# Kernel optimization log

Measured on AMD Instinct MI355X. Metric: run time of the kernel, lower is better.

Reference implementation:

```python
import jax, jax.numpy as jnp
import numpy as np

B, N, C, K, OUT = 4, 16384, 64, 16, 128
BN_EPS = 1e-5


def setup_inputs() -> dict:
    key = jax.random.key(0)
    ks = jax.random.split(key, 6)
    feature = jax.random.normal(ks[0], (B, C, N), dtype=jnp.float32)
    neigh_index = jax.random.randint(ks[1], (B * N, K), 0, B * N)
    permatrix = jnp.zeros((1,), dtype=jnp.float32)  # unused by forward
    # Conv1d(in_c, in_c, kernel_size=1, bias=False) -> weight [C, C]
    W_mlp = jax.random.normal(ks[2], (C, C), dtype=jnp.float32) / np.sqrt(C).astype(np.float32)
    # Linear(in_c, out_c) -> weight [OUT, C], bias [OUT]
    W_conv = jax.random.normal(ks[3], (OUT, C), dtype=jnp.float32) / np.sqrt(C).astype(np.float32)
    b_conv = jax.random.normal(ks[4], (OUT,), dtype=jnp.float32) * 0.01
    gamma = jnp.ones((OUT,), dtype=jnp.float32)
    beta = jnp.zeros((OUT,), dtype=jnp.float32)
    return {
        "feature": feature,
        "neigh_index": neigh_index,
        "permatrix": permatrix,
        "W_mlp": W_mlp,
        "W_conv": W_conv,
        "b_conv": b_conv,
        "gamma": gamma,
        "beta": beta,
    }


def reference(feature, neigh_index, permatrix, W_mlp, W_conv, b_conv, gamma, beta):
    bsize, feats, num_pts = feature.shape
    # [B, C, N] -> [B*N, C]
    flat = feature.transpose(0, 2, 1).reshape(bsize * num_pts, feats)
    # irregular gather: [B*N, k, C]
    spirals = flat[neigh_index]
    # 1x1 conv over channels: einsum with mlp weight [C_out=C, C_in=C]
    scores = jnp.einsum("nkc,dc->nkd", spirals, W_mlp)  # [B*N, k, C]
    # softmax over channel dim (torch dim=1 on [BN, C, k] layout)
    attn = jax.nn.softmax(scores, axis=-1)
    # attention pooling over the k neighbors -> [B*N, C]
    pooled = jnp.sum(attn * spirals, axis=1)
    # Linear: [B*N, OUT]
    out = pooled @ W_conv.T + b_conv
    # [B, OUT, N]
    out = out.reshape(bsize, num_pts, -1).transpose(0, 2, 1)
    # BatchNorm1d (training-mode batch statistics) over (batch, points) per channel
    mean = jnp.mean(out, axis=(0, 2), keepdims=True)
    var = jnp.var(out, axis=(0, 2), keepdims=True)
    out = (out - mean) * jax.lax.rsqrt(var + BN_EPS)
    out = out * gamma[None, :, None] + beta[None, :, None]
    return out
```

## Files before the change

### kernel.cpp

```cpp
#include <hip/hip_runtime.h>
#include <cstdint>

#define NPTS   16384
#define BATCH  4
#define BNP    65536
#define CIN    64
#define KNB    16
#define COUT   128
#define BN_EPS 1e-5f

typedef __attribute__((ext_vector_type(8))) short     short8;
typedef __attribute__((ext_vector_type(4))) float     f32x4;
typedef __attribute__((ext_vector_type(2))) unsigned  u32x2;
typedef __attribute__((ext_vector_type(4))) int       i32x4;

__device__ __forceinline__ unsigned short f2bf(float f) {
    unsigned u = __float_as_uint(f);
    u += 0x7FFFu + ((u >> 16) & 1u);
    return (unsigned short)(u >> 16);
}
__device__ __forceinline__ float bf2f(unsigned short h) {
    return __uint_as_float(((unsigned)h) << 16);
}

__global__ __launch_bounds__(256) void k_prep(const float* __restrict__ feat,
                                              unsigned short* __restrict__ fb,
                                              const float* __restrict__ Wm,
                                              const float* __restrict__ Wc,
                                              unsigned short* __restrict__ wmb,
                                              unsigned short* __restrict__ wcb)
{
    if (blockIdx.x == 1024) {
        #pragma unroll
        for (int i = threadIdx.x; i < CIN * CIN; i += 256)       wmb[i] = f2bf(Wm[i]);
        #pragma unroll
        for (int i = threadIdx.x; i < COUT * CIN; i += 256)      wcb[i] = f2bf(Wc[i]);
        return;
    }
    __shared__ float t[CIN][CIN + 1];
    int blk = blockIdx.x;
    int b   = blk >> 8;
    int n0  = (blk & 255) << 6;
    int sub = threadIdx.x >> 6, lane = threadIdx.x & 63;
    const float* fp = feat + (size_t)b * CIN * NPTS;
    #pragma unroll
    for (int r = 0; r < CIN; r += 4) {
        int c = r + sub;
        t[c][lane] = fp[(size_t)c * NPTS + n0 + lane];
    }
    __syncthreads();
    unsigned short* ob = fb + (size_t)(b * NPTS + n0) * CIN;
    #pragma unroll
    for (int r = 0; r < CIN; r += 4) {
        int x = r + sub;
        ob[(size_t)x * CIN + lane] = f2bf(t[lane][x]);
    }
}

__global__ __launch_bounds__(256, 2) void k_main(
    const unsigned short* __restrict__ fb,
    const int* __restrict__ nidx,
    const unsigned short* __restrict__ wmb,
    const unsigned short* __restrict__ wcb,
    float* __restrict__ out)
{
    __shared__ __align__(16) unsigned short plds[4][2][1152];

    const int tid  = threadIdx.x;
    const int wv   = tid >> 6;
    const int lane = tid & 63;
    const int ptc  = lane & 15;
    const int qg   = lane >> 4;
    const int p4   = ptc * 4;

    short8 wmF[4][2];
    #pragma unroll
    for (int mt = 0; mt < 4; ++mt)
        #pragma unroll
        for (int ks = 0; ks < 2; ++ks)
            wmF[mt][ks] = *(const short8*)&wmb[(size_t)(mt * 16 + ptc) * CIN + qg * 8 + ks * 32];
    short8 wcF[8][2];
    #pragma unroll
    for (int mt = 0; mt < 8; ++mt)
        #pragma unroll
        for (int ks = 0; ks < 2; ++ks)
            wcF[mt][ks] = *(const short8*)&wcb[(size_t)(mt * 16 + ptc) * CIN + qg * 8 + ks * 32];

    f32x4 acc2[8];
    #pragma unroll
    for (int i = 0; i < 8; ++i) acc2[i] = (f32x4){0.f, 0.f, 0.f, 0.f};

    const int g = blockIdx.x * 4 + wv;

    i32x4 iv = *(const i32x4*)(nidx + (size_t)g * 256 + lane * 4);

    short8 rb0[4], rb1[4];
    u32x2  svr[4][4];
    int    rid[4];
    #pragma unroll
    for (int kk = 0; kk < 4; ++kk) {
        int id = __shfl(iv[kk], p4);
        rid[kk] = id;
        const unsigned short* gp = fb + (size_t)id * CIN;
        rb0[kk] = *(const short8*)(gp + qg * 8);
        rb1[kk] = *(const short8*)(gp + 32 + qg * 8);
        #pragma unroll
        for (int mt = 0; mt < 4; ++mt)
            svr[kk][mt] = *(const u32x2*)(gp + mt * 16 + qg * 4);
    }

    #pragma unroll
    for (int p = 0; p < 8; ++p) {
        const int sA = (2 * p) & 3;
        const int sB = sA + 1;

        f32x4 zero4 = (f32x4){0.f, 0.f, 0.f, 0.f};
        f32x4 a1A[4], a1B[4];
        #pragma unroll
        for (int mt = 0; mt < 4; ++mt) {
            f32x4 t0 = __builtin_amdgcn_mfma_f32_16x16x32_bf16(wmF[mt][0], rb0[sA], zero4, 0, 0, 0);
            a1A[mt]  = __builtin_amdgcn_mfma_f32_16x16x32_bf16(wmF[mt][1], rb1[sA], t0,    0, 0, 0);
        }
        #pragma unroll
        for (int mt = 0; mt < 4; ++mt) {
            f32x4 t0 = __builtin_amdgcn_mfma_f32_16x16x32_bf16(wmF[mt][0], rb0[sB], zero4, 0, 0, 0);
            a1B[mt]  = __builtin_amdgcn_mfma_f32_16x16x32_bf16(wmF[mt][1], rb1[sB], t0,    0, 0, 0);
        }

        if (p < 6) {
            int idA = __shfl(iv[sA], p4 + ((2 * p + 4) >> 2));
            int idB = __shfl(iv[sB], p4 + ((2 * p + 5) >> 2));
            rid[sA] = idA;
            rid[sB] = idB;
            const unsigned short* gA = fb + (size_t)idA * CIN;
            const unsigned short* gB = fb + (size_t)idB * CIN;
            rb0[sA] = *(const short8*)(gA + qg * 8);
            rb1[sA] = *(const short8*)(gA + 32 + qg * 8);
            rb0[sB] = *(const short8*)(gB + qg * 8);
            rb1[sB] = *(const short8*)(gB + 32 + qg * 8);
        }

        float ssA = 0.f, ssB = 0.f;
        #pragma unroll
        for (int mt = 0; mt < 4; ++mt)
            #pragma unroll
            for (int r = 0; r < 4; ++r) {
                float xA = __expf(a1A[mt][r]);
                float xB = __expf(a1B[mt][r]);
                a1A[mt][r] = xA;  ssA += xA;
                a1B[mt][r] = xB;  ssB += xB;
            }
        ssA += __shfl_xor(ssA, 16);
        ssB += __shfl_xor(ssB, 16);
        ssA += __shfl_xor(ssA, 32);
        ssB += __shfl_xor(ssB, 32);
        float invA = __builtin_amdgcn_rcpf(ssA);
        float invB = __builtin_amdgcn_rcpf(ssB);

        #pragma unroll
        for (int mt = 0; mt < 4; ++mt) {
            u32x2 svA = svr[sA][mt], svB = svr[sB][mt];
            unsigned loA = svA[0], hiA = svA[1];
            unsigned loB = svB[0], hiB = svB[1];
            float pA0 = bf2f((unsigned short)loA)         * (a1A[mt][0] * invA);
            float pA1 = bf2f((unsigned short)(loA >> 16)) * (a1A[mt][1] * invA);
            float pA2 = bf2f((unsigned short)hiA)         * (a1A[mt][2] * invA);
            float pA3 = bf2f((unsigned short)(hiA >> 16)) * (a1A[mt][3] * invA);
            float pB0 = bf2f((unsigned short)loB)         * (a1B[mt][0] * invB);
            float pB1 = bf2f((unsigned short)(loB >> 16)) * (a1B[mt][1] * invB);
            float pB2 = bf2f((unsigned short)hiB)         * (a1B[mt][2] * invB);
            float pB3 = bf2f((unsigned short)(hiB >> 16)) * (a1B[mt][3] * invB);
            unsigned wA0 = ((__float_as_uint(pA0) + 0x8000u) >> 16) |
                           ((__float_as_uint(pA1) + 0x8000u) & 0xFFFF0000u);
            unsigned wA1 = ((__float_as_uint(pA2) + 0x8000u) >> 16) |
                           ((__float_as_uint(pA3) + 0x8000u) & 0xFFFF0000u);
            unsigned wB0 = ((__float_as_uint(pB0) + 0x8000u) >> 16) |
                           ((__float_as_uint(pB1) + 0x8000u) & 0xFFFF0000u);
            unsigned wB1 = ((__float_as_uint(pB2) + 0x8000u) >> 16) |
                           ((__float_as_uint(pB3) + 0x8000u) & 0xFFFF0000u);
            *(u32x2*)&plds[wv][0][ptc * 72 + mt * 16 + qg * 4] = (u32x2){wA0, wA1};
            *(u32x2*)&plds[wv][1][ptc * 72 + mt * 16 + qg * 4] = (u32x2){wB0, wB1};
        }

        if (p < 6) {
            const unsigned short* gA = fb + (size_t)rid[sA] * CIN;
            const unsigned short* gB = fb + (size_t)rid[sB] * CIN;
            #pragma unroll
            for (int mt = 0; mt < 4; ++mt) {
                svr[sA][mt] = *(const u32x2*)(gA + mt * 16 + qg * 4);
                svr[sB][mt] = *(const u32x2*)(gB + mt * 16 + qg * 4);
            }
        }

        short8 b2A0 = *(const short8*)&plds[wv][0][ptc * 72 +      qg * 8];
        short8 b2A1 = *(const short8*)&plds[wv][0][ptc * 72 + 32 + qg * 8];
        short8 b2B0 = *(const short8*)&plds[wv][1][ptc * 72 +      qg * 8];
        short8 b2B1 = *(const short8*)&plds[wv][1][ptc * 72 + 32 + qg * 8];

        #pragma unroll
        for (int mt = 0; mt < 8; ++mt) {
            acc2[mt] = __builtin_amdgcn_mfma_f32_16x16x32_bf16(wcF[mt][0], b2A0, acc2[mt], 0, 0, 0);
            acc2[mt] = __builtin_amdgcn_mfma_f32_16x16x32_bf16(wcF[mt][1], b2A1, acc2[mt], 0, 0, 0);
        }
        #pragma unroll
        for (int mt = 0; mt < 8; ++mt) {
            acc2[mt] = __builtin_amdgcn_mfma_f32_16x16x32_bf16(wcF[mt][0], b2B0, acc2[mt], 0, 0, 0);
            acc2[mt] = __builtin_amdgcn_mfma_f32_16x16x32_bf16(wcF[mt][1], b2B1, acc2[mt], 0, 0, 0);
        }
    }

    {
        int p0 = g * KNB;
        int b  = p0 >> 14;
        int nn = (p0 & (NPTS - 1)) + ptc;
        float* ob = out + (((size_t)b * COUT) << 14) + nn;
        #pragma unroll
        for (int mt = 0; mt < 8; ++mt)
            #pragma unroll
            for (int r = 0; r < 4; ++r)
                ob[((size_t)(mt * 16 + qg * 4 + r)) << 14] = acc2[mt][r];
    }
}

__global__ __launch_bounds__(256) void k_part(const float* __restrict__ out,
                                              float* __restrict__ part)
{
    int o = blockIdx.x >> 2, b = blockIdx.x & 3;
    const float4* p = (const float4*)(out + (((size_t)(b * COUT + o)) << 14));
    float s = 0.f, q = 0.f;
    for (int i = threadIdx.x; i < NPTS / 4; i += 256) {
        float4 v = p[i];
        s += (v.x + v.y) + (v.z + v.w);
        q += (v.x * v.x + v.y * v.y) + (v.z * v.z + v.w * v.w);
    }
    #pragma unroll
    for (int off = 32; off >= 1; off >>= 1) {
        s += __shfl_xor(s, off);
        q += __shfl_xor(q, off);
    }
    __shared__ float ls[4], lq[4];
    if ((threadIdx.x & 63) == 0) { ls[threadIdx.x >> 6] = s; lq[threadIdx.x >> 6] = q; }
    __syncthreads();
    if (threadIdx.x == 0) {
        part[blockIdx.x * 2]     = (ls[0] + ls[1]) + (ls[2] + ls[3]);
        part[blockIdx.x * 2 + 1] = (lq[0] + lq[1]) + (lq[2] + lq[3]);
    }
}

__global__ __launch_bounds__(256) void k_apply(float* __restrict__ out,
                                               const float* __restrict__ part,
                                               const float* __restrict__ gamma,
                                               const float* __restrict__ beta)
{
    __shared__ float sc[COUT], sh[COUT];
    int t = threadIdx.x;
    if (t < COUT) {
        float s = 0.f, q = 0.f;
        #pragma unroll
        for (int j = 0; j < 4; ++j) {
            s += part[(t * 4 + j) * 2];
            q += part[(t * 4 + j) * 2 + 1];
        }
        float mean = s * (1.0f / BNP);
        float var  = q * (1.0f / BNP) - mean * mean;
        float a = gamma[t] * rsqrtf(var + BN_EPS);
        sc[t] = a; sh[t] = beta[t] - mean * a;
    }
    __syncthreads();
    const int total4 = BATCH * COUT * NPTS / 4;
    for (long i = (long)blockIdx.x * 256 + t; i < total4; i += (long)gridDim.x * 256) {
        int ch = ((int)(i >> 12)) & 127;
        float4 v = ((float4*)out)[i];
        float a = sc[ch], b2 = sh[ch];
        v.x = fmaf(v.x, a, b2); v.y = fmaf(v.y, a, b2);
        v.z = fmaf(v.z, a, b2); v.w = fmaf(v.w, a, b2);
        ((float4*)out)[i] = v;
    }
}

extern "C" void kernel_launch(void* const* d_in, const int* in_sizes, int n_in,
                              void* d_out, int out_size, void* d_ws, size_t ws_size,
                              hipStream_t stream)
{
    const float* feat  = (const float*)d_in[0];
    const int*   nidx  = (const int*)  d_in[1];
    const float* Wm    = (const float*)d_in[3];
    const float* Wc    = (const float*)d_in[4];
    const float* gamma = (const float*)d_in[6];
    const float* beta  = (const float*)d_in[7];
    float* out = (float*)d_out;

    char* ws = (char*)d_ws;
    unsigned short* fb   = (unsigned short*)ws;
    float*          part = (float*)(ws + (size_t)BNP * CIN * 2);
    unsigned short* wmb  = (unsigned short*)(ws + (size_t)BNP * CIN * 2 + 4096);
    unsigned short* wcb  = wmb + CIN * CIN;

    k_prep <<<1025, 256, 0, stream>>>(feat, fb, Wm, Wc, wmb, wcb);
    k_main <<<1024, 256, 0, stream>>>(fb, nidx, wmb, wcb, out);
    k_part <<<512,  256, 0, stream>>>(out, part);
    k_apply<<<2048, 256, 0, stream>>>(out, part, gamma, beta);
}
```

Before: 165.5 us.

## Fuse BatchNorm statistics into main kernel via shuffle reduction and atomics

```diff
diff --git a/kernel.cpp b/kernel.cpp
--- a/kernel.cpp
+++ b/kernel.cpp
@@ -28,9 +28,11 @@
                                               const float* __restrict__ Wm,
                                               const float* __restrict__ Wc,
                                               unsigned short* __restrict__ wmb,
-                                              unsigned short* __restrict__ wcb)
+                                              unsigned short* __restrict__ wcb,
+                                              float* __restrict__ stat)
 {
     if (blockIdx.x == 1024) {
+        stat[threadIdx.x] = 0.f;
         #pragma unroll
         for (int i = threadIdx.x; i < CIN * CIN; i += 256)       wmb[i] = f2bf(Wm[i]);
         #pragma unroll
@@ -62,7 +64,8 @@
     const int* __restrict__ nidx,
     const unsigned short* __restrict__ wmb,
     const unsigned short* __restrict__ wcb,
-    float* __restrict__ out)
+    float* __restrict__ out,
+    float* __restrict__ stat)
 {
     __shared__ __align__(16) unsigned short plds[4][2][1152];
 
@@ -220,49 +223,37 @@
             for (int r = 0; r < 4; ++r)
                 ob[((size_t)(mt * 16 + qg * 4 + r)) << 14] = acc2[mt][r];
     }
-}
-
-__global__ __launch_bounds__(256) void k_part(const float* __restrict__ out,
-                                              float* __restrict__ part)
-{
-    int o = blockIdx.x >> 2, b = blockIdx.x & 3;
-    const float4* p = (const float4*)(out + (((size_t)(b * COUT + o)) << 14));
-    float s = 0.f, q = 0.f;
-    for (int i = threadIdx.x; i < NPTS / 4; i += 256) {
-        float4 v = p[i];
-        s += (v.x + v.y) + (v.z + v.w);
-        q += (v.x * v.x + v.y * v.y) + (v.z * v.z + v.w * v.w);
-    }
-    #pragma unroll
-    for (int off = 32; off >= 1; off >>= 1) {
-        s += __shfl_xor(s, off);
-        q += __shfl_xor(q, off);
-    }
-    __shared__ float ls[4], lq[4];
-    if ((threadIdx.x & 63) == 0) { ls[threadIdx.x >> 6] = s; lq[threadIdx.x >> 6] = q; }
-    __syncthreads();
-    if (threadIdx.x == 0) {
-        part[blockIdx.x * 2]     = (ls[0] + ls[1]) + (ls[2] + ls[3]);
-        part[blockIdx.x * 2 + 1] = (lq[0] + lq[1]) + (lq[2] + lq[3]);
-    }
+
+    #pragma unroll
+    for (int mt = 0; mt < 8; ++mt)
+        #pragma unroll
+        for (int r = 0; r < 4; ++r) {
+            float v = acc2[mt][r];
+            float s = v, q = v * v;
+            #pragma unroll
+            for (int m = 1; m <= 8; m <<= 1) {
+                s += __shfl_xor(s, m);
+                q += __shfl_xor(q, m);
+            }
+            if (ptc == 0) {
+                int ch = mt * 16 + qg * 4 + r;
+                atomicAdd(&stat[ch],        s);
+                atomicAdd(&stat[COUT + ch], q);
+            }
+        }
 }
 
 __global__ __launch_bounds__(256) void k_apply(float* __restrict__ out,
-                                               const float* __restrict__ part,
+                                               const float* __restrict__ stat,
                                                const float* __restrict__ gamma,
                                                const float* __restrict__ beta)
 {
     __shared__ float sc[COUT], sh[COUT];
     int t = threadIdx.x;
     if (t < COUT) {
-        float s = 0.f, q = 0.f;
-        #pragma unroll
-        for (int j = 0; j < 4; ++j) {
-            s += part[(t * 4 + j) * 2];
-            q += part[(t * 4 + j) * 2 + 1];
-        }
-        float mean = s * (1.0f / BNP);
-        float var  = q * (1.0f / BNP) - mean * mean;
+        float S = stat[t], Q = stat[COUT + t];
+        float mean = S * (1.0f / BNP);
+        float var  = Q * (1.0f / BNP) - mean * mean;
         float a = gamma[t] * rsqrtf(var + BN_EPS);
         sc[t] = a; sh[t] = beta[t] - mean * a;
     }
@@ -292,12 +283,11 @@
 
     char* ws = (char*)d_ws;
     unsigned short* fb   = (unsigned short*)ws;
-    float*          part = (float*)(ws + (size_t)BNP * CIN * 2);
-    unsigned short* wmb  = (unsigned short*)(ws + (size_t)BNP * CIN * 2 + 4096);
+    float*          stat = (float*)(ws + (size_t)BNP * CIN * 2);
+    unsigned short* wmb  = (unsigned short*)(ws + (size_t)BNP * CIN * 2 + 1024);
     unsigned short* wcb  = wmb + CIN * CIN;
 
-    k_prep <<<1025, 256, 0, stream>>>(feat, fb, Wm, Wc, wmb, wcb);
-    k_main <<<1024, 256, 0, stream>>>(fb, nidx, wmb, wcb, out);
-    k_part <<<512,  256, 0, stream>>>(out, part);
-    k_apply<<<2048, 256, 0, stream>>>(out, part, gamma, beta);
-}
+    k_prep <<<1025, 256, 0, stream>>>(feat, fb, Wm, Wc, wmb, wcb, stat);
+    k_main <<<1024, 256, 0, stream>>>(fb, nidx, wmb, wcb, out, stat);
+    k_apply<<<2048, 256, 0, stream>>>(out, stat, gamma, beta);
+}
```

Result: slower. 570.5 us (+244.7%).

## Fuse prep, main, stats and BN apply into one cooperative persistent kernel

Applied to the files above, without the earlier changes.

```diff
diff --git a/kernel.cpp b/kernel.cpp
--- a/kernel.cpp
+++ b/kernel.cpp
@@ -1,5 +1,8 @@
 #include <hip/hip_runtime.h>
+#include <hip/hip_cooperative_groups.h>
 #include <cstdint>
+
+namespace cg = cooperative_groups;
 
 #define NPTS   16384
 #define BATCH  4
@@ -21,6 +24,254 @@
 }
 __device__ __forceinline__ float bf2f(unsigned short h) {
     return __uint_as_float(((unsigned)h) << 16);
+}
+
+__global__ __launch_bounds__(256, 2) void k_fused(
+    const float* __restrict__ feat, const int* __restrict__ nidx,
+    const float* __restrict__ Wm,   const float* __restrict__ Wc,
+    const float* __restrict__ gamma, const float* __restrict__ beta,
+    float* __restrict__ out, unsigned short* __restrict__ fb,
+    unsigned short* __restrict__ wmb, unsigned short* __restrict__ wcb,
+    float* __restrict__ part)
+{
+    __shared__ float tl[CIN][CIN + 1];
+    __shared__ __align__(16) unsigned short plds[4][2][1152];
+    __shared__ float sc[COUT], sh[COUT];
+    __shared__ float ls[4], lq[4];
+
+    const int tid  = threadIdx.x;
+    const int wv   = tid >> 6;
+    const int lane = tid & 63;
+
+    {
+        #pragma clang loop unroll(disable)
+        for (int t2 = 0; t2 < 2; ++t2) {
+            int blk = blockIdx.x * 2 + t2;
+            int b = blk >> 8, n0 = (blk & 255) << 6;
+            const float* fp = feat + (size_t)b * CIN * NPTS;
+            #pragma unroll
+            for (int r = 0; r < CIN; r += 4) {
+                int c = r + wv;
+                tl[c][lane] = fp[(size_t)c * NPTS + n0 + lane];
+            }
+            __syncthreads();
+            unsigned short* ob = fb + (size_t)(b * NPTS + n0) * CIN;
+            #pragma unroll
+            for (int r = 0; r < CIN; r += 4) {
+                int x = r + wv;
+                ob[(size_t)x * CIN + lane] = f2bf(tl[lane][x]);
+            }
+            __syncthreads();
+        }
+        if (blockIdx.x == 0) {
+            for (int i = tid; i < CIN * CIN; i += 256)  wmb[i] = f2bf(Wm[i]);
+            for (int i = tid; i < COUT * CIN; i += 256) wcb[i] = f2bf(Wc[i]);
+        }
+    }
+    cg::this_grid().sync();
+
+    {
+        const int ptc = lane & 15;
+        const int qg  = lane >> 4;
+        const int p4  = ptc * 4;
+
+        short8 wmF[4][2];
+        #pragma unroll
+        for (int mt = 0; mt < 4; ++mt)
+            #pragma unroll
+            for (int ks = 0; ks < 2; ++ks)
+                wmF[mt][ks] = *(const short8*)&wmb[(size_t)(mt * 16 + ptc) * CIN + qg * 8 + ks * 32];
+        short8 wcF[8][2];
+        #pragma unroll
+        for (int mt = 0; mt < 8; ++mt)
+            #pragma unroll
+            for (int ks = 0; ks < 2; ++ks)
+                wcF[mt][ks] = *(const short8*)&wcb[(size_t)(mt * 16 + ptc) * CIN + qg * 8 + ks * 32];
+
+        f32x4 acc2[8];
+        #pragma unroll
+        for (int i = 0; i < 8; ++i) acc2[i] = (f32x4){0.f, 0.f, 0.f, 0.f};
+
+        for (int g = blockIdx.x * 4 + wv; g < BNP / KNB; g += 2048) {
+            i32x4 iv = *(const i32x4*)(nidx + (size_t)g * 256 + lane * 4);
+
+            short8 rb0[4], rb1[4];
+            u32x2  svr[4][4];
+            int    rid[4];
+            #pragma unroll
+            for (int kk = 0; kk < 4; ++kk) {
+                int id = __shfl(iv[kk], p4);
+                rid[kk] = id;
+                const unsigned short* gp = fb + (size_t)id * CIN;
+                rb0[kk] = *(const short8*)(gp + qg * 8);
+                rb1[kk] = *(const short8*)(gp + 32 + qg * 8);
+                #pragma unroll
+                for (int mt = 0; mt < 4; ++mt)
+                    svr[kk][mt] = *(const u32x2*)(gp + mt * 16 + qg * 4);
+            }
+
+            #pragma unroll
+            for (int p = 0; p < 8; ++p) {
+                const int sA = (2 * p) & 3;
+                const int sB = sA + 1;
+
+                f32x4 zero4 = (f32x4){0.f, 0.f, 0.f, 0.f};
+                f32x4 a1A[4], a1B[4];
+                #pragma unroll
+                for (int mt = 0; mt < 4; ++mt) {
+                    f32x4 t0 = __builtin_amdgcn_mfma_f32_16x16x32_bf16(wmF[mt][0], rb0[sA], zero4, 0, 0, 0);
+                    a1A[mt]  = __builtin_amdgcn_mfma_f32_16x16x32_bf16(wmF[mt][1], rb1[sA], t0,    0, 0, 0);
+                }
+                #pragma unroll
+                for (int mt = 0; mt < 4; ++mt) {
+                    f32x4 t0 = __builtin_amdgcn_mfma_f32_16x16x32_bf16(wmF[mt][0], rb0[sB], zero4, 0, 0, 0);
+                    a1B[mt]  = __builtin_amdgcn_mfma_f32_16x16x32_bf16(wmF[mt][1], rb1[sB], t0,    0, 0, 0);
+                }
+
+                if (p < 6) {
+                    int idA = __shfl(iv[sA], p4 + ((2 * p + 4) >> 2));
+                    int idB = __shfl(iv[sB], p4 + ((2 * p + 5) >> 2));
+                    rid[sA] = idA;
+                    rid[sB] = idB;
+                    const unsigned short* gA = fb + (size_t)idA * CIN;
+                    const unsigned short* gB = fb + (size_t)idB * CIN;
+                    rb0[sA] = *(const short8*)(gA + qg * 8);
+                    rb1[sA] = *(const short8*)(gA + 32 + qg * 8);
+                    rb0[sB] = *(const short8*)(gB + qg * 8);
+                    rb1[sB] = *(const short8*)(gB + 32 + qg * 8);
+                }
+
+                float ssA = 0.f, ssB = 0.f;
+                #pragma unroll
+                for (int mt = 0; mt < 4; ++mt)
+                    #pragma unroll
+                    for (int r = 0; r < 4; ++r) {
+                        float xA = __expf(a1A[mt][r]);
+                        float xB = __expf(a1B[mt][r]);
+                        a1A[mt][r] = xA;  ssA += xA;
+                        a1B[mt][r] = xB;  ssB += xB;
+                    }
+                ssA += __shfl_xor(ssA, 16);
+                ssB += __shfl_xor(ssB, 16);
+                ssA += __shfl_xor(ssA, 32);
+                ssB += __shfl_xor(ssB, 32);
+                float invA = __builtin_amdgcn_rcpf(ssA);
+                float invB = __builtin_amdgcn_rcpf(ssB);
+
+                #pragma unroll
+                for (int mt = 0; mt < 4; ++mt) {
+                    u32x2 svA = svr[sA][mt], svB = svr[sB][mt];
+                    unsigned loA = svA[0], hiA = svA[1];
+                    unsigned loB = svB[0], hiB = svB[1];
+                    float pA0 = bf2f((unsigned short)loA)         * (a1A[mt][0] * invA);
+                    float pA1 = bf2f((unsigned short)(loA >> 16)) * (a1A[mt][1] * invA);
+                    float pA2 = bf2f((unsigned short)hiA)         * (a1A[mt][2] * invA);
+                    float pA3 = bf2f((unsigned short)(hiA >> 16)) * (a1A[mt][3] * invA);
+                    float pB0 = bf2f((unsigned short)loB)         * (a1B[mt][0] * invB);
+                    float pB1 = bf2f((unsigned short)(loB >> 16)) * (a1B[mt][1] * invB);
+                    float pB2 = bf2f((unsigned short)hiB)         * (a1B[mt][2] * invB);
+                    float pB3 = bf2f((unsigned short)(hiB >> 16)) * (a1B[mt][3] * invB);
+                    unsigned wA0 = ((__float_as_uint(pA0) + 0x8000u) >> 16) |
+                                   ((__float_as_uint(pA1) + 0x8000u) & 0xFFFF0000u);
+                    unsigned wA1 = ((__float_as_uint(pA2) + 0x8000u) >> 16) |
+                                   ((__float_as_uint(pA3) + 0x8000u) & 0xFFFF0000u);
+                    unsigned wB0 = ((__float_as_uint(pB0) + 0x8000u) >> 16) |
+                                   ((__float_as_uint(pB1) + 0x8000u) & 0xFFFF0000u);
+                    unsigned wB1 = ((__float_as_uint(pB2) + 0x8000u) >> 16) |
+                                   ((__float_as_uint(pB3) + 0x8000u) & 0xFFFF0000u);
+                    *(u32x2*)&plds[wv][0][ptc * 72 + mt * 16 + qg * 4] = (u32x2){wA0, wA1};
+                    *(u32x2*)&plds[wv][1][ptc * 72 + mt * 16 + qg * 4] = (u32x2){wB0, wB1};
+                }
+
+                if (p < 6) {
+                    const unsigned short* gA = fb + (size_t)rid[sA] * CIN;
+                    const unsigned short* gB = fb + (size_t)rid[sB] * CIN;
+                    #pragma unroll
+                    for (int mt = 0; mt < 4; ++mt) {
+                        svr[sA][mt] = *(const u32x2*)(gA + mt * 16 + qg * 4);
+                        svr[sB][mt] = *(const u32x2*)(gB + mt * 16 + qg * 4);
+                    }
+                }
+
+                short8 b2A0 = *(const short8*)&plds[wv][0][ptc * 72 +      qg * 8];
+                short8 b2A1 = *(const short8*)&plds[wv][0][ptc * 72 + 32 + qg * 8];
+                short8 b2B0 = *(const short8*)&plds[wv][1][ptc * 72 +      qg * 8];
+                short8 b2B1 = *(const short8*)&plds[wv][1][ptc * 72 + 32 + qg * 8];
+
+                #pragma unroll
+                for (int mt = 0; mt < 8; ++mt) {
+                    acc2[mt] = __builtin_amdgcn_mfma_f32_16x16x32_bf16(wcF[mt][0], b2A0, acc2[mt], 0, 0, 0);
+                    acc2[mt] = __builtin_amdgcn_mfma_f32_16x16x32_bf16(wcF[mt][1], b2A1, acc2[mt], 0, 0, 0);
+                }
+                #pragma unroll
+                for (int mt = 0; mt < 8; ++mt) {
+                    acc2[mt] = __builtin_amdgcn_mfma_f32_16x16x32_bf16(wcF[mt][0], b2B0, acc2[mt], 0, 0, 0);
+                    acc2[mt] = __builtin_amdgcn_mfma_f32_16x16x32_bf16(wcF[mt][1], b2B1, acc2[mt], 0, 0, 0);
+                }
+            }
+
+            int p0 = g * KNB;
+            int b  = p0 >> 14;
+            int nn = (p0 & (NPTS - 1)) + ptc;
+            float* ob = out + (((size_t)b * COUT) << 14) + nn;
+            #pragma unroll
+            for (int mt = 0; mt < 8; ++mt)
+                #pragma unroll
+                for (int r = 0; r < 4; ++r) {
+                    ob[((size_t)(mt * 16 + qg * 4 + r)) << 14] = acc2[mt][r];
+                    acc2[mt][r] = 0.f;
+                }
+        }
+    }
+    cg::this_grid().sync();
+
+    {
+        int o = blockIdx.x >> 2, b = blockIdx.x & 3;
+        const float4* pp = (const float4*)(out + (((size_t)(b * COUT + o)) << 14));
+        float s = 0.f, q = 0.f;
+        for (int i = tid; i < NPTS / 4; i += 256) {
+            float4 v = pp[i];
+            s += (v.x + v.y) + (v.z + v.w);
+            q += (v.x * v.x + v.y * v.y) + (v.z * v.z + v.w * v.w);
+        }
+        #pragma unroll
+        for (int off = 32; off >= 1; off >>= 1) {
+            s += __shfl_xor(s, off);
+            q += __shfl_xor(q, off);
+        }
+        if (lane == 0) { ls[wv] = s; lq[wv] = q; }
+        __syncthreads();
+        if (tid == 0) {
+            part[blockIdx.x * 2]     = (ls[0] + ls[1]) + (ls[2] + ls[3]);
+            part[blockIdx.x * 2 + 1] = (lq[0] + lq[1]) + (lq[2] + lq[3]);
+        }
+    }
+    cg::this_grid().sync();
+
+    {
+        if (tid < COUT) {
+            float s = 0.f, q = 0.f;
+            #pragma unroll
+            for (int j = 0; j < 4; ++j) {
+                s += part[(tid * 4 + j) * 2];
+                q += part[(tid * 4 + j) * 2 + 1];
+            }
+            float mean = s * (1.0f / BNP);
+            float var  = q * (1.0f / BNP) - mean * mean;
+            float a = gamma[tid] * rsqrtf(var + BN_EPS);
+            sc[tid] = a; sh[tid] = beta[tid] - mean * a;
+        }
+        __syncthreads();
+        const int total4 = BATCH * COUT * NPTS / 4;
+        for (long i = (long)blockIdx.x * 256 + tid; i < total4; i += (long)gridDim.x * 256) {
+            int ch = ((int)(i >> 12)) & 127;
+            float4 v = ((float4*)out)[i];
+            float a = sc[ch], b2 = sh[ch];
+            v.x = fmaf(v.x, a, b2); v.y = fmaf(v.y, a, b2);
+            v.z = fmaf(v.z, a, b2); v.w = fmaf(v.w, a, b2);
+            ((float4*)out)[i] = v;
+        }
+    }
 }
 
 __global__ __launch_bounds__(256) void k_prep(const float* __restrict__ feat,
@@ -58,14 +309,11 @@
 }
 
 __global__ __launch_bounds__(256, 2) void k_main(
-    const unsigned short* __restrict__ fb,
-    const int* __restrict__ nidx,
-    const unsigned short* __restrict__ wmb,
-    const unsigned short* __restrict__ wcb,
+    const unsigned short* __restrict__ fb, const int* __restrict__ nidx,
+    const unsigned short* __restrict__ wmb, const unsigned short* __restrict__ wcb,
     float* __restrict__ out)
 {
     __shared__ __align__(16) unsigned short plds[4][2][1152];
-
     const int tid  = threadIdx.x;
     const int wv   = tid >> 6;
     const int lane = tid & 63;
@@ -91,7 +339,6 @@
     for (int i = 0; i < 8; ++i) acc2[i] = (f32x4){0.f, 0.f, 0.f, 0.f};
 
     const int g = blockIdx.x * 4 + wv;
-
     i32x4 iv = *(const i32x4*)(nidx + (size_t)g * 256 + lane * 4);
 
     short8 rb0[4], rb1[4];
@@ -113,7 +360,6 @@
     for (int p = 0; p < 8; ++p) {
         const int sA = (2 * p) & 3;
         const int sB = sA + 1;
-
         f32x4 zero4 = (f32x4){0.f, 0.f, 0.f, 0.f};
         f32x4 a1A[4], a1B[4];
         #pragma unroll
@@ -126,7 +372,6 @@
             f32x4 t0 = __builtin_amdgcn_mfma_f32_16x16x32_bf16(wmF[mt][0], rb0[sB], zero4, 0, 0, 0);
             a1B[mt]  = __builtin_amdgcn_mfma_f32_16x16x32_bf16(wmF[mt][1], rb1[sB], t0,    0, 0, 0);
         }
-
         if (p < 6) {
             int idA = __shfl(iv[sA], p4 + ((2 * p + 4) >> 2));
             int idB = __shfl(iv[sB], p4 + ((2 * p + 5) >> 2));
@@ -139,7 +384,6 @@
             rb0[sB] = *(const short8*)(gB + qg * 8);
             rb1[sB] = *(const short8*)(gB + 32 + qg * 8);
         }
-
         float ssA = 0.f, ssB = 0.f;
         #pragma unroll
         for (int mt = 0; mt < 4; ++mt)
@@ -156,7 +400,6 @@
         ssB += __shfl_xor(ssB, 32);
         float invA = __builtin_amdgcn_rcpf(ssA);
         float invB = __builtin_amdgcn_rcpf(ssB);
-
         #pragma unroll
         for (int mt = 0; mt < 4; ++mt) {
             u32x2 svA = svr[sA][mt], svB = svr[sB][mt];
@@ -181,7 +424,6 @@
             *(u32x2*)&plds[wv][0][ptc * 72 + mt * 16 + qg * 4] = (u32x2){wA0, wA1};
             *(u32x2*)&plds[wv][1][ptc * 72 + mt * 16 + qg * 4] = (u32x2){wB0, wB1};
         }
-
         if (p < 6) {
             const unsigned short* gA = fb + (size_t)rid[sA] * CIN;
             const unsigned short* gB = fb + (size_t)rid[sB] * CIN;
@@ -191,12 +433,10 @@
                 svr[sB][mt] = *(const u32x2*)(gB + mt * 16 + qg * 4);
             }
         }
-
         short8 b2A0 = *(const short8*)&plds[wv][0][ptc * 72 +      qg * 8];
         short8 b2A1 = *(const short8*)&plds[wv][0][ptc * 72 + 32 + qg * 8];
         short8 b2B0 = *(const short8*)&plds[wv][1][ptc * 72 +      qg * 8];
         short8 b2B1 = *(const short8*)&plds[wv][1][ptc * 72 + 32 + qg * 8];
-
         #pragma unroll
         for (int mt = 0; mt < 8; ++mt) {
             acc2[mt] = __builtin_amdgcn_mfma_f32_16x16x32_bf16(wcF[mt][0], b2A0, acc2[mt], 0, 0, 0);
@@ -209,17 +449,15 @@
         }
     }
 
-    {
-        int p0 = g * KNB;
-        int b  = p0 >> 14;
-        int nn = (p0 & (NPTS - 1)) + ptc;
-        float* ob = out + (((size_t)b * COUT) << 14) + nn;
-        #pragma unroll
-        for (int mt = 0; mt < 8; ++mt)
-            #pragma unroll
-            for (int r = 0; r < 4; ++r)
-                ob[((size_t)(mt * 16 + qg * 4 + r)) << 14] = acc2[mt][r];
-    }
+    int p0 = g * KNB;
+    int b  = p0 >> 14;
+    int nn = (p0 & (NPTS - 1)) + ptc;
+    float* ob = out + (((size_t)b * COUT) << 14) + nn;
+    #pragma unroll
+    for (int mt = 0; mt < 8; ++mt)
+        #pragma unroll
+        for (int r = 0; r < 4; ++r)
+            ob[((size_t)(mt * 16 + qg * 4 + r)) << 14] = acc2[mt][r];
 }
 
 __global__ __launch_bounds__(256) void k_part(const float* __restrict__ out,
@@ -296,8 +534,18 @@
     unsigned short* wmb  = (unsigned short*)(ws + (size_t)BNP * CIN * 2 + 4096);
     unsigned short* wcb  = wmb + CIN * CIN;
 
-    k_prep <<<1025, 256, 0, stream>>>(feat, fb, Wm, Wc, wmb, wcb);
-    k_main <<<1024, 256, 0, stream>>>(fb, nidx, wmb, wcb, out);
-    k_part <<<512,  256, 0, stream>>>(out, part);
-    k_apply<<<2048, 256, 0, stream>>>(out, part, gamma, beta);
-}
+    void* args[] = {
+        (void*)&feat, (void*)&nidx, (void*)&Wm, (void*)&Wc,
+        (void*)&gamma, (void*)&beta, (void*)&out,
+        (void*)&fb, (void*)&wmb, (void*)&wcb, (void*)&part
+    };
+    hipError_t e = hipLaunchCooperativeKernel((const void*)k_fused,
+                                              dim3(512), dim3(256), args, 0, stream);
+    if (e != hipSuccess) {
+        (void)hipGetLastError();
+        k_prep <<<1025, 256, 0, stream>>>(feat, fb, Wm, Wc, wmb, wcb);
+        k_main <<<1024, 256, 0, stream>>>(fb, nidx, wmb, wcb, out);
+        k_part <<<512,  256, 0, stream>>>(out, part);
+        k_apply<<<2048, 256, 0, stream>>>(out, part, gamma, beta);
+    }
+}
```

Result: slower. 361.9 us (+118.7%).
